# Performance work log

Measured on AMD Instinct MI355X. Metric: run time of the kernel, lower is better.

The kernel has to match this reference:

```python
import jax, jax.numpy as jnp
import numpy as np

E = 512   # embed_dim
H = 512   # hidden_embed_dim
V = 50257 # vocab_size
B = 2048  # batch
EPS = 1e-5


def _layernorm(v, gamma, beta):
    # PyTorch LayerNorm with normalized_shape=(1, H): normalize over last two dims
    m = jnp.mean(v, axis=(-2, -1), keepdims=True)
    var = jnp.var(v, axis=(-2, -1), keepdims=True)
    return (v - m) * jax.lax.rsqrt(var + EPS) * gamma + beta


def setup_inputs() -> dict:
    key = jax.random.key(0)
    ks = jax.random.split(key, 12)
    s_in = 1.0 / np.sqrt(E + H)
    s_h = 1.0 / np.sqrt(H)
    return {
        "x": jax.random.normal(ks[0], (B, 1, E), jnp.float32),
        "h_prev": jax.random.normal(ks[1], (B, 1, H), jnp.float32),
        "W_z": jax.random.normal(ks[2], (H, E + H), jnp.float32) * s_in,
        "b_z": jnp.zeros((H,), jnp.float32),
        "g_z": jnp.ones((1, H), jnp.float32),
        "be_z": jnp.zeros((1, H), jnp.float32),
        "W_r": jax.random.normal(ks[3], (H, E + H), jnp.float32) * s_in,
        "b_r": jnp.zeros((H,), jnp.float32),
        "g_r": jnp.ones((1, H), jnp.float32),
        "be_r": jnp.zeros((1, H), jnp.float32),
        "W_h": jax.random.normal(ks[4], (H, E + H), jnp.float32) * s_in,
        "b_h": jnp.zeros((H,), jnp.float32),
        "g_h": jnp.ones((1, H), jnp.float32),
        "be_h": jnp.zeros((1, H), jnp.float32),
        "W_o": jax.random.normal(ks[5], (V, H), jnp.float32) * s_h,
        "b_o": jnp.zeros((V,), jnp.float32),
    }


def reference(x, h_prev, W_z, b_z, g_z, be_z, W_r, b_r, g_r, be_r,
              W_h, b_h, g_h, be_h, W_o, b_o):
    gru_in = jnp.concatenate([h_prev, x], axis=-1)                 # [B,1,H+E]
    z = jax.nn.sigmoid(_layernorm(gru_in @ W_z.T + b_z, g_z, be_z))
    r = jax.nn.sigmoid(_layernorm(gru_in @ W_r.T + b_r, g_r, be_r))
    cand_in = jnp.concatenate([h_prev * r, x], axis=-1)            # [B,1,H+E]
    h_new = jnp.tanh(_layernorm(cand_in @ W_h.T + b_h, g_h, be_h))
    h_t = (1.0 - z) * h_prev + z * h_new                           # [B,1,H]
    y_t = h_t @ W_o.T + b_o                                        # [B,1,V]
    return (h_t, y_t)
```

## Files before the change

### kernel.cpp

```cpp
#include <hip/hip_runtime.h>
#include <hip/hip_bf16.h>
#include <cstdint>

typedef __bf16 bf16;
typedef bf16 bf16x4 __attribute__((ext_vector_type(4)));
typedef bf16 bf16x8 __attribute__((ext_vector_type(8)));
typedef float f32x4 __attribute__((ext_vector_type(4)));

#define B_  2048
#define E_  512
#define H_  512
#define V_  50257
#define K1_ 1024
#define VPAD_ 50432

#define BAR() __builtin_amdgcn_s_barrier()
#define WAIT_LGKM0() do { asm volatile("s_waitcnt lgkmcnt(0)" ::: "memory"); \
                          __builtin_amdgcn_sched_barrier(0); } while (0)

__device__ __forceinline__ void gload_lds16(const void* g, void* l) {
  __builtin_amdgcn_global_load_lds(
      (const __attribute__((address_space(1))) void*)g,
      (__attribute__((address_space(3))) void*)l, 16, 0, 0);
}

__device__ __forceinline__ float wave_sum(float v) {
#pragma unroll
  for (int o = 32; o > 0; o >>= 1) v += __shfl_xor(v, o, 64);
  return v;
}

__global__ __launch_bounds__(256) void prep_big_kernel(
    const float* __restrict__ hprev, const float* __restrict__ x,
    const float* __restrict__ Wz, const float* __restrict__ Wr,
    const float* __restrict__ Wh, const float* __restrict__ Wo,
    bf16* __restrict__ gin, bf16* __restrict__ wzrh, bf16* __restrict__ wob)
{
  const int i = blockIdx.x * 256 + threadIdx.x;
  constexpr int N1 = B_ * K1_ / 4;
  constexpr int N2 = 1536 * K1_ / 4;
  constexpr int N3 = V_ * 512 / 4;
  if (i < N1) {
    int e = i * 4;
    int m = e >> 10, k = e & 1023;
    const float* src = (k < 512) ? (hprev + (size_t)m * 512 + k)
                                 : (x + (size_t)m * 512 + (k - 512));
    f32x4 v = *reinterpret_cast<const f32x4*>(src);
    bf16x4 t; t[0]=(bf16)v[0]; t[1]=(bf16)v[1]; t[2]=(bf16)v[2]; t[3]=(bf16)v[3];
    *reinterpret_cast<bf16x4*>(gin + e) = t;
  } else if (i < N1 + N2) {
    int e = (i - N1) * 4;
    int which = e >> 19;
    int off = e & ((1 << 19) - 1);
    const float* W = (which == 0) ? Wz : (which == 1) ? Wr : Wh;
    f32x4 v = *reinterpret_cast<const f32x4*>(W + off);
    bf16x4 t; t[0]=(bf16)v[0]; t[1]=(bf16)v[1]; t[2]=(bf16)v[2]; t[3]=(bf16)v[3];
    *reinterpret_cast<bf16x4*>(wzrh + e) = t;
  } else if (i < N1 + N2 + N3) {
    size_t e = (size_t)(i - N1 - N2) * 4;
    f32x4 v = *reinterpret_cast<const f32x4*>(Wo + e);
    bf16x4 t; t[0]=(bf16)v[0]; t[1]=(bf16)v[1]; t[2]=(bf16)v[2]; t[3]=(bf16)v[3];
    *reinterpret_cast<bf16x4*>(wob + e) = t;
  } else {
    size_t e = (size_t)V_ * 512 + (size_t)(i - N1 - N2 - N3) * 4;
    bf16x4 t = {};
    *reinterpret_cast<bf16x4*>(wob + e) = t;
  }
}

__global__ __launch_bounds__(256) void gemm64(
    const bf16* __restrict__ A, const bf16* __restrict__ Bm,
    float* __restrict__ C, int M, int N, int K)
{
  __shared__ bf16 As[2][64 * 64];
  __shared__ bf16 Bs[2][128 * 64];
  const int tid = threadIdx.x;
  const int wid = tid >> 6, lane = tid & 63;
  const int bm = blockIdx.x, bn = blockIdx.y;
  const int wm = (wid >> 1) * 32, wn = (wid & 1) * 64;
  f32x4 acc[2][4] = {};
  const size_t a_row0 = (size_t)bm * 64;
  const size_t b_row0 = (size_t)bn * 128;

  auto STAGE = [&](int buf, int k0) {
#pragma unroll
    for (int i = 0; i < 2; ++i) {
      int base = i * 256 + wid * 64;
      int idx = base + lane;
      int row = idx >> 3;
      int col = ((idx & 7) ^ (row & 7)) << 3;
      gload_lds16(A + (a_row0 + row) * K + (k0 + col), &As[buf][base * 8]);
    }
#pragma unroll
    for (int i = 0; i < 4; ++i) {
      int base = i * 256 + wid * 64;
      int idx = base + lane;
      int row = idx >> 3;
      int col = ((idx & 7) ^ (row & 7)) << 3;
      gload_lds16(Bm + (b_row0 + row) * K + (k0 + col), &Bs[buf][base * 8]);
    }
  };

  auto COMPUTE = [&](int buf) {
#pragma unroll
    for (int kk = 0; kk < 2; ++kk) {
      bf16x8 af[2], bb[4];
#pragma unroll
      for (int i = 0; i < 2; ++i) {
        int ra = wm + i * 16 + (lane & 15);
        int ca = (kk * 32 + (lane >> 4) * 8) ^ ((ra & 7) << 3);
        af[i] = *reinterpret_cast<const bf16x8*>(&As[buf][ra * 64 + ca]);
      }
#pragma unroll
      for (int j = 0; j < 4; ++j) {
        int rb = wn + j * 16 + (lane & 15);
        int cb = (kk * 32 + (lane >> 4) * 8) ^ ((rb & 7) << 3);
        bb[j] = *reinterpret_cast<const bf16x8*>(&Bs[buf][rb * 64 + cb]);
      }
      __builtin_amdgcn_s_setprio(1);
#pragma unroll
      for (int i = 0; i < 2; ++i)
#pragma unroll
        for (int j = 0; j < 4; ++j)
          acc[i][j] = __builtin_amdgcn_mfma_f32_16x16x32_bf16(af[i], bb[j], acc[i][j], 0, 0, 0);
      __builtin_amdgcn_s_setprio(0);
    }
  };

  STAGE(0, 0);
  asm volatile("s_waitcnt vmcnt(0)" ::: "memory");
  __syncthreads();
  const int nt = K >> 6;
  int cur = 0;
  for (int t = 0; t < nt - 1; ++t) {
    STAGE(cur ^ 1, (t + 1) << 6);
    COMPUTE(cur);
    asm volatile("s_waitcnt vmcnt(0)" ::: "memory");
    __syncthreads();
    cur ^= 1;
  }
  COMPUTE(cur);

  const int r0 = (lane >> 4) * 4, cc = lane & 15;
#pragma unroll
  for (int i = 0; i < 2; ++i)
#pragma unroll
    for (int j = 0; j < 4; ++j) {
      int n = bn * 128 + wn + j * 16 + cc;
#pragma unroll
      for (int q = 0; q < 4; ++q) {
        int mm = bm * 64 + wm + i * 16 + r0 + q;
        C[(size_t)mm * N + n] = acc[i][j][q];
      }
    }
}

__global__ __launch_bounds__(256) void ln_zr_kernel(
    const float* __restrict__ zrp,
    const float* __restrict__ bz, const float* __restrict__ br,
    const float* __restrict__ gz, const float* __restrict__ bez,
    const float* __restrict__ gr, const float* __restrict__ ber,
    const float* __restrict__ hprev, const float* __restrict__ x,
    float* __restrict__ zbuf, bf16* __restrict__ cand)
{
  const int m = blockIdx.x, tid = threadIdx.x;
  const int wid = tid >> 6, lane = tid & 63;
  float zv[2], rv[2];
  float s0 = 0, s1 = 0, s2 = 0, s3 = 0;
#pragma unroll
  for (int e = 0; e < 2; ++e) {
    int n = tid + e * 256;
    float a = zrp[(size_t)m * 1024 + n] + bz[n];
    float b = zrp[(size_t)m * 1024 + 512 + n] + br[n];
    zv[e] = a; rv[e] = b;
    s0 += a; s1 += a * a; s2 += b; s3 += b * b;
  }
  s0 = wave_sum(s0); s1 = wave_sum(s1); s2 = wave_sum(s2); s3 = wave_sum(s3);
  __shared__ float red[4][4];
  if (lane == 0) { red[wid][0] = s0; red[wid][1] = s1; red[wid][2] = s2; red[wid][3] = s3; }
  __syncthreads();
  float zs = red[0][0] + red[1][0] + red[2][0] + red[3][0];
  float zq = red[0][1] + red[1][1] + red[2][1] + red[3][1];
  float rs = red[0][2] + red[1][2] + red[2][2] + red[3][2];
  float rq = red[0][3] + red[1][3] + red[2][3] + red[3][3];
  float zm = zs * (1.f / 512.f), zvr = zq * (1.f / 512.f) - zm * zm;
  float rm = rs * (1.f / 512.f), rvr = rq * (1.f / 512.f) - rm * rm;
  float zrs_ = rsqrtf(zvr + 1e-5f), rrs = rsqrtf(rvr + 1e-5f);
#pragma unroll
  for (int e = 0; e < 2; ++e) {
    int n = tid + e * 256;
    float zval = 1.f / (1.f + expf(-((zv[e] - zm) * zrs_ * gz[n] + bez[n])));
    float rval = 1.f / (1.f + expf(-((rv[e] - rm) * rrs * gr[n] + ber[n])));
    zbuf[(size_t)m * 512 + n] = zval;
    cand[(size_t)m * 1024 + n] = (bf16)(hprev[(size_t)m * 512 + n] * rval);
    cand[(size_t)m * 1024 + 512 + n] = (bf16)(x[(size_t)m * 512 + n]);
  }
}

__global__ __launch_bounds__(256) void ln_h_kernel(
    const float* __restrict__ hpre, const float* __restrict__ bh,
    const float* __restrict__ gh, const float* __restrict__ beh,
    const float* __restrict__ zbuf, const float* __restrict__ hprev,
    float* __restrict__ outh, bf16* __restrict__ htb)
{
  const int m = blockIdx.x, tid = threadIdx.x;
  const int wid = tid >> 6, lane = tid & 63;
  float v[2];
  float s0 = 0, s1 = 0;
#pragma unroll
  for (int e = 0; e < 2; ++e) {
    int n = tid + e * 256;
    float a = hpre[(size_t)m * 512 + n] + bh[n];
    v[e] = a; s0 += a; s1 += a * a;
  }
  s0 = wave_sum(s0); s1 = wave_sum(s1);
  __shared__ float red[4][2];
  if (lane == 0) { red[wid][0] = s0; red[wid][1] = s1; }
  __syncthreads();
  float ss = red[0][0] + red[1][0] + red[2][0] + red[3][0];
  float sq = red[0][1] + red[1][1] + red[2][1] + red[3][1];
  float mean = ss * (1.f / 512.f), var = sq * (1.f / 512.f) - mean * mean;
  float rstd = rsqrtf(var + 1e-5f);
#pragma unroll
  for (int e = 0; e < 2; ++e) {
    int n = tid + e * 256;
    float hn = tanhf((v[e] - mean) * rstd * gh[n] + beh[n]);
    float z = zbuf[(size_t)m * 512 + n];
    float ht = (1.f - z) * hprev[(size_t)m * 512 + n] + z * hn;
    outh[(size_t)m * 512 + n] = ht;
    htb[(size_t)m * 512 + n] = (bf16)ht;
  }
}

__global__ __launch_bounds__(512, 2) void gemm_out256(
    const bf16* __restrict__ A, const bf16* __restrict__ Wb,
    const float* __restrict__ bo, float* __restrict__ Y)
{
  __shared__ bf16 lds[2][2][2][128 * 64];
  const int tid = threadIdx.x;
  const int lane = tid & 63;
  const int wid = tid >> 6;
  const int wr = wid >> 2, wc = wid & 3;
  const int hw = blockIdx.x;
  const int logical = (hw & 7) * 197 + (hw >> 3);
  const int bm = logical & 7;
  const int bn = logical >> 3;
  const size_t a_row0 = (size_t)bm * 256;
  const size_t b_row0 = (size_t)bn * 256;
  f32x4 acc[8][4] = {};

  auto STAGE = [&](int p, int op, int h, int ks) {
    const bf16* src = op ? Wb : A;
    const size_t r0 = (op ? b_row0 : a_row0) + h * 128;
    const int k0 = ks << 6;
#pragma unroll
    for (int l = 0; l < 2; ++l) {
      int idx = l * 512 + tid;
      int row = idx >> 3;
      int ch = ((idx & 7) ^ (row & 7)) << 3;
      gload_lds16(src + (r0 + row) * 512 + k0 + ch,
                  &lds[p][op][h][(l * 512 + (tid & ~63)) * 8]);
    }
  };

  auto rdA = [&](int p, int i, int kk) -> bf16x8 {
    int lr = i * 16 + (lane & 15);
    int ch = ((kk * 4 + (lane >> 4)) ^ (lr & 7)) << 3;
    return *reinterpret_cast<const bf16x8*>(&lds[p][0][wr][lr * 64 + ch]);
  };
  auto rdB = [&](int p, int j, int kk) -> bf16x8 {
    int gr = wc * 64 + j * 16 + (lane & 15);
    int lr = gr & 127;
    int ch = ((kk * 4 + (lane >> 4)) ^ (lr & 7)) << 3;
    return *reinterpret_cast<const bf16x8*>(&lds[p][1][wc >> 1][lr * 64 + ch]);
  };

  bf16x8 a0[4][2], a1[4][2], bb0[2][2], bb1[2][2];

  auto MM = [&](bf16x8 (&af)[4][2], bf16x8 (&bf)[2][2], int ib, int jb) {
    __builtin_amdgcn_s_setprio(1);
#pragma unroll
    for (int i = 0; i < 4; ++i)
#pragma unroll
      for (int j = 0; j < 2; ++j)
#pragma unroll
        for (int kk = 0; kk < 2; ++kk)
          acc[ib + i][jb + j] =
              __builtin_amdgcn_mfma_f32_16x16x32_bf16(af[i][kk], bf[j][kk],
                                                      acc[ib + i][jb + j], 0, 0, 0);
    __builtin_amdgcn_s_setprio(0);
  };

  STAGE(0, 0, 0, 0); STAGE(0, 0, 1, 0); STAGE(0, 1, 0, 0); STAGE(0, 1, 1, 0);
  STAGE(1, 0, 0, 1); STAGE(1, 0, 1, 1);
  asm volatile("s_waitcnt vmcnt(4)" ::: "memory");
  BAR();

#pragma unroll 1
  for (int it = 0; it < 4; ++it) {
    const int s = 2 * it;
    const bool pre = (it < 3);
#pragma unroll
    for (int i = 0; i < 4; ++i) { a0[i][0] = rdA(0, i, 0); a0[i][1] = rdA(0, i, 1); }
#pragma unroll
    for (int j = 0; j < 2; ++j) { bb0[j][0] = rdB(0, j, 0); bb0[j][1] = rdB(0, j, 1); }
    STAGE(1, 1, 0, s + 1);
    BAR(); WAIT_LGKM0();
    MM(a0, bb0, 0, 0);
    BAR();
#pragma unroll
    for (int i = 0; i < 4; ++i) { a1[i][0] = rdA(0, 4 + i, 0); a1[i][1] = rdA(0, 4 + i, 1); }
    STAGE(1, 1, 1, s + 1);
    BAR(); WAIT_LGKM0();
    MM(a1, bb0, 4, 0);
    BAR();
#pragma unroll
    for (int j = 0; j < 2; ++j) { bb1[j][0] = rdB(0, 2 + j, 0); bb1[j][1] = rdB(0, 2 + j, 1); }
    if (pre) STAGE(0, 0, 0, s + 2);
    BAR(); WAIT_LGKM0();
    MM(a0, bb1, 0, 2);
    BAR();
    if (pre) { STAGE(0, 1, 0, s + 2);
               asm volatile("s_waitcnt vmcnt(4)" ::: "memory"); }
    else     { asm volatile("s_waitcnt vmcnt(0)" ::: "memory"); }
    BAR();
    MM(a1, bb1, 4, 2);
    BAR();
#pragma unroll
    for (int i = 0; i < 4; ++i) { a0[i][0] = rdA(1, i, 0); a0[i][1] = rdA(1, i, 1); }
#pragma unroll
    for (int j = 0; j < 2; ++j) { bb0[j][0] = rdB(1, j, 0); bb0[j][1] = rdB(1, j, 1); }
    if (pre) STAGE(0, 0, 1, s + 2);
    BAR(); WAIT_LGKM0();
    MM(a0, bb0, 0, 0);
    BAR();
#pragma unroll
    for (int i = 0; i < 4; ++i) { a1[i][0] = rdA(1, 4 + i, 0); a1[i][1] = rdA(1, 4 + i, 1); }
    if (pre) STAGE(0, 1, 1, s + 2);
    BAR(); WAIT_LGKM0();
    MM(a1, bb0, 4, 0);
    BAR();
#pragma unroll
    for (int j = 0; j < 2; ++j) { bb1[j][0] = rdB(1, 2 + j, 0); bb1[j][1] = rdB(1, 2 + j, 1); }
    if (pre) STAGE(1, 0, 0, s + 3);
    BAR(); WAIT_LGKM0();
    MM(a0, bb1, 0, 2);
    BAR();
    if (pre) { STAGE(1, 0, 1, s + 3);
               asm volatile("s_waitcnt vmcnt(4)" ::: "memory"); }
    BAR();
    MM(a1, bb1, 4, 2);
    BAR();
  }

  const int r0q = (lane >> 4) * 4, cc = lane & 15;
  const int rowbase = (int)a_row0 + wr * 128;
  const int colbase = (int)b_row0 + wc * 64;
  float bia[4]; bool val[4];
#pragma unroll
  for (int j = 0; j < 4; ++j) {
    int n = colbase + j * 16 + cc;
    val[j] = (n < V_);
    bia[j] = val[j] ? bo[n] : 0.f;
  }
#pragma unroll
  for (int i = 0; i < 8; ++i) {
#pragma unroll
    for (int q = 0; q < 4; ++q) {
      size_t rowoff = (size_t)(rowbase + i * 16 + r0q + q) * V_;
#pragma unroll
      for (int j = 0; j < 4; ++j) {
        if (val[j]) Y[rowoff + colbase + j * 16 + cc] = acc[i][j][q] + bia[j];
      }
    }
  }
}

__global__ __launch_bounds__(256) void gemm_out_kernel(
    const bf16* __restrict__ A, const float* __restrict__ Wo,
    const float* __restrict__ bo, float* __restrict__ Y)
{
  __shared__ bf16 As[128 * 64];
  __shared__ bf16 Bs[128 * 64];
  constexpr int K = 512;
  const int tid = threadIdx.x;
  const int wid = tid >> 6, lane = tid & 63;
  const int bm = blockIdx.x, bn = blockIdx.y;
  const int wm = (wid >> 1) * 64, wn = (wid & 1) * 64;
  f32x4 acc[4][4] = {};

  for (int k0 = 0; k0 < K; k0 += 64) {
#pragma unroll
    for (int i = 0; i < 4; ++i) {
      int base = i * 256 + wid * 64;
      int idx = base + lane;
      int row = idx >> 3, col = (idx & 7) << 3;
      gload_lds16(A + ((size_t)bm * 128 + row) * K + (k0 + col), &As[base * 8]);
    }
#pragma unroll
    for (int i = 0; i < 8; ++i) {
      int idx = i * 256 + tid;
      int row = idx >> 4;
      int c4 = (idx & 15) * 4;
      int n = bn * 128 + row;
      int nc = (n < V_) ? n : (V_ - 1);
      f32x4 v = *reinterpret_cast<const f32x4*>(Wo + (size_t)nc * K + k0 + c4);
      bf16x4 t; t[0]=(bf16)v[0]; t[1]=(bf16)v[1]; t[2]=(bf16)v[2]; t[3]=(bf16)v[3];
      *reinterpret_cast<bf16x4*>(&Bs[row * 64 + c4]) = t;
    }
    asm volatile("s_waitcnt vmcnt(0)" ::: "memory");
    __syncthreads();
#pragma unroll
    for (int kk = 0; kk < 2; ++kk) {
      bf16x8 af[4], bb[4];
#pragma unroll
      for (int i = 0; i < 4; ++i)
        af[i] = *reinterpret_cast<const bf16x8*>(
            &As[(wm + i * 16 + (lane & 15)) * 64 + kk * 32 + (lane >> 4) * 8]);
#pragma unroll
      for (int j = 0; j < 4; ++j)
        bb[j] = *reinterpret_cast<const bf16x8*>(
            &Bs[(wn + j * 16 + (lane & 15)) * 64 + kk * 32 + (lane >> 4) * 8]);
#pragma unroll
      for (int i = 0; i < 4; ++i)
#pragma unroll
        for (int j = 0; j < 4; ++j)
          acc[i][j] = __builtin_amdgcn_mfma_f32_16x16x32_bf16(af[i], bb[j], acc[i][j], 0, 0, 0);
    }
    __syncthreads();
  }

  const int r0 = (lane >> 4) * 4, cc = lane & 15;
#pragma unroll
  for (int i = 0; i < 4; ++i)
#pragma unroll
    for (int j = 0; j < 4; ++j) {
      int n = bn * 128 + wn + j * 16 + cc;
      if (n < V_) {
        float bia = bo[n];
#pragma unroll
        for (int q = 0; q < 4; ++q) {
          int mm = bm * 128 + wm + i * 16 + r0 + q;
          Y[(size_t)mm * V_ + n] = acc[i][j][q] + bia;
        }
      }
    }
}

__global__ __launch_bounds__(256) void prep_kernel(
    const float* __restrict__ hprev, const float* __restrict__ x,
    const float* __restrict__ Wz, const float* __restrict__ Wr,
    const float* __restrict__ Wh,
    bf16* __restrict__ gin, bf16* __restrict__ wzrh)
{
  const int i = blockIdx.x * 256 + threadIdx.x;
  constexpr int N1 = B_ * K1_ / 4;
  constexpr int N2 = 1536 * K1_ / 4;
  if (i < N1) {
    int e = i * 4;
    int m = e >> 10, k = e & 1023;
    const float* src = (k < 512) ? (hprev + (size_t)m * 512 + k)
                                 : (x + (size_t)m * 512 + (k - 512));
    f32x4 v = *reinterpret_cast<const f32x4*>(src);
    bf16x4 t; t[0]=(bf16)v[0]; t[1]=(bf16)v[1]; t[2]=(bf16)v[2]; t[3]=(bf16)v[3];
    *reinterpret_cast<bf16x4*>(gin + e) = t;
  } else if (i < N1 + N2) {
    int e = (i - N1) * 4;
    int which = e >> 19;
    int off = e & ((1 << 19) - 1);
    const float* W = (which == 0) ? Wz : (which == 1) ? Wr : Wh;
    f32x4 v = *reinterpret_cast<const f32x4*>(W + off);
    bf16x4 t; t[0]=(bf16)v[0]; t[1]=(bf16)v[1]; t[2]=(bf16)v[2]; t[3]=(bf16)v[3];
    *reinterpret_cast<bf16x4*>(wzrh + e) = t;
  }
}

extern "C" void kernel_launch(void* const* d_in, const int* in_sizes, int n_in,
                              void* d_out, int out_size, void* d_ws, size_t ws_size,
                              hipStream_t stream) {
  const float* x     = (const float*)d_in[0];
  const float* hprev = (const float*)d_in[1];
  const float* Wz    = (const float*)d_in[2];
  const float* bz    = (const float*)d_in[3];
  const float* gz    = (const float*)d_in[4];
  const float* bez   = (const float*)d_in[5];
  const float* Wr    = (const float*)d_in[6];
  const float* br    = (const float*)d_in[7];
  const float* gr    = (const float*)d_in[8];
  const float* ber   = (const float*)d_in[9];
  const float* Wh    = (const float*)d_in[10];
  const float* bh    = (const float*)d_in[11];
  const float* gh    = (const float*)d_in[12];
  const float* beh   = (const float*)d_in[13];
  const float* Wo    = (const float*)d_in[14];
  const float* bo    = (const float*)d_in[15];

  float* out_h = (float*)d_out;
  float* out_y = out_h + (size_t)B_ * H_;

  char* ws = (char*)d_ws;
  bf16*  gin  = (bf16*)(ws);
  bf16*  wzrh = (bf16*)(ws + ((size_t)4 << 20));
  float* zrp  = (float*)(ws + ((size_t)7 << 20));
  float* zbuf = (float*)(ws + ((size_t)15 << 20));
  bf16*  cand = (bf16*)(ws + ((size_t)19 << 20));
  float* hpre = (float*)(ws + ((size_t)23 << 20));
  bf16*  htb  = (bf16*)(ws + ((size_t)27 << 20));
  bf16*  wob  = (bf16*)(ws + ((size_t)29 << 20));

  constexpr size_t NEED = ((size_t)29 << 20) + (size_t)VPAD_ * 512 * 2;

  if (ws_size >= NEED) {
    prep_big_kernel<<<28800, 256, 0, stream>>>(hprev, x, Wz, Wr, Wh, Wo, gin, wzrh, wob);
  } else {
    prep_kernel<<<3584, 256, 0, stream>>>(hprev, x, Wz, Wr, Wh, gin, wzrh);
  }

  gemm64<<<dim3(32, 8), 256, 0, stream>>>(gin, wzrh, zrp, B_, 1024, K1_);
  ln_zr_kernel<<<B_, 256, 0, stream>>>(zrp, bz, br, gz, bez, gr, ber, hprev, x, zbuf, cand);
  gemm64<<<dim3(32, 4), 256, 0, stream>>>(cand, wzrh + (size_t)1024 * 1024, hpre, B_, 512, K1_);
  ln_h_kernel<<<B_, 256, 0, stream>>>(hpre, bh, gh, beh, zbuf, hprev, out_h, htb);

  if (ws_size >= NEED) {
    gemm_out256<<<1576, 512, 0, stream>>>(htb, wob, bo, out_y);
  } else {
    gemm_out_kernel<<<dim3(16, 393), 256, 0, stream>>>(htb, Wo, bo, out_y);
  }
}
```

Measured before the change: 317.8 us.

## Overlap W_o bf16 conversion with gate GEMM and LN kernels via extra blocks

The large fp32-to-bf16 conversion of W_o is removed from the prep kernel and split into two halves. One half is done by extra blocks appended to the z/r gate GEMM launch, the other by extra blocks appended to the z/r LayerNorm launch. The aim is to hide this bandwidth-heavy conversion behind the small, underutilising early kernels instead of running it serially up front. The catch is that the added blocks may contend for memory bandwidth and delay the critical-path GEMM and LN work.

```diff
diff --git a/kernel.cpp b/kernel.cpp
--- a/kernel.cpp
+++ b/kernel.cpp
@@ -14,6 +14,10 @@
 #define K1_ 1024
 #define VPAD_ 50432
 
+#define CONV_TOT  6432896
+#define CONV_PAD  6455296
+#define CONV_HALF 3216448
+
 #define BAR() __builtin_amdgcn_s_barrier()
 #define WAIT_LGKM0() do { asm volatile("s_waitcnt lgkmcnt(0)" ::: "memory"); \
                           __builtin_amdgcn_sched_barrier(0); } while (0)
@@ -30,421 +34,11 @@
   return v;
 }
 
-__global__ __launch_bounds__(256) void prep_big_kernel(
-    const float* __restrict__ hprev, const float* __restrict__ x,
-    const float* __restrict__ Wz, const float* __restrict__ Wr,
-    const float* __restrict__ Wh, const float* __restrict__ Wo,
-    bf16* __restrict__ gin, bf16* __restrict__ wzrh, bf16* __restrict__ wob)
-{
-  const int i = blockIdx.x * 256 + threadIdx.x;
-  constexpr int N1 = B_ * K1_ / 4;
-  constexpr int N2 = 1536 * K1_ / 4;
-  constexpr int N3 = V_ * 512 / 4;
-  if (i < N1) {
-    int e = i * 4;
-    int m = e >> 10, k = e & 1023;
-    const float* src = (k < 512) ? (hprev + (size_t)m * 512 + k)
-                                 : (x + (size_t)m * 512 + (k - 512));
-    f32x4 v = *reinterpret_cast<const f32x4*>(src);
-    bf16x4 t; t[0]=(bf16)v[0]; t[1]=(bf16)v[1]; t[2]=(bf16)v[2]; t[3]=(bf16)v[3];
-    *reinterpret_cast<bf16x4*>(gin + e) = t;
-  } else if (i < N1 + N2) {
-    int e = (i - N1) * 4;
-    int which = e >> 19;
-    int off = e & ((1 << 19) - 1);
-    const float* W = (which == 0) ? Wz : (which == 1) ? Wr : Wh;
-    f32x4 v = *reinterpret_cast<const f32x4*>(W + off);
-    bf16x4 t; t[0]=(bf16)v[0]; t[1]=(bf16)v[1]; t[2]=(bf16)v[2]; t[3]=(bf16)v[3];
-    *reinterpret_cast<bf16x4*>(wzrh + e) = t;
-  } else if (i < N1 + N2 + N3) {
-    size_t e = (size_t)(i - N1 - N2) * 4;
-    f32x4 v = *reinterpret_cast<const f32x4*>(Wo + e);
-    bf16x4 t; t[0]=(bf16)v[0]; t[1]=(bf16)v[1]; t[2]=(bf16)v[2]; t[3]=(bf16)v[3];
-    *reinterpret_cast<bf16x4*>(wob + e) = t;
-  } else {
-    size_t e = (size_t)V_ * 512 + (size_t)(i - N1 - N2 - N3) * 4;
-    bf16x4 t = {};
-    *reinterpret_cast<bf16x4*>(wob + e) = t;
-  }
-}
-
-__global__ __launch_bounds__(256) void gemm64(
-    const bf16* __restrict__ A, const bf16* __restrict__ Bm,
-    float* __restrict__ C, int M, int N, int K)
-{
-  __shared__ bf16 As[2][64 * 64];
-  __shared__ bf16 Bs[2][128 * 64];
-  const int tid = threadIdx.x;
-  const int wid = tid >> 6, lane = tid & 63;
-  const int bm = blockIdx.x, bn = blockIdx.y;
-  const int wm = (wid >> 1) * 32, wn = (wid & 1) * 64;
-  f32x4 acc[2][4] = {};
-  const size_t a_row0 = (size_t)bm * 64;
-  const size_t b_row0 = (size_t)bn * 128;
-
-  auto STAGE = [&](int buf, int k0) {
-#pragma unroll
-    for (int i = 0; i < 2; ++i) {
-      int base = i * 256 + wid * 64;
-      int idx = base + lane;
-      int row = idx >> 3;
-      int col = ((idx & 7) ^ (row & 7)) << 3;
-      gload_lds16(A + (a_row0 + row) * K + (k0 + col), &As[buf][base * 8]);
-    }
-#pragma unroll
-    for (int i = 0; i < 4; ++i) {
-      int base = i * 256 + wid * 64;
-      int idx = base + lane;
-      int row = idx >> 3;
-      int col = ((idx & 7) ^ (row & 7)) << 3;
-      gload_lds16(Bm + (b_row0 + row) * K + (k0 + col), &Bs[buf][base * 8]);
-    }
-  };
-
-  auto COMPUTE = [&](int buf) {
-#pragma unroll
-    for (int kk = 0; kk < 2; ++kk) {
-      bf16x8 af[2], bb[4];
-#pragma unroll
-      for (int i = 0; i < 2; ++i) {
-        int ra = wm + i * 16 + (lane & 15);
-        int ca = (kk * 32 + (lane >> 4) * 8) ^ ((ra & 7) << 3);
-        af[i] = *reinterpret_cast<const bf16x8*>(&As[buf][ra * 64 + ca]);
-      }
-#pragma unroll
-      for (int j = 0; j < 4; ++j) {
-        int rb = wn + j * 16 + (lane & 15);
-        int cb = (kk * 32 + (lane >> 4) * 8) ^ ((rb & 7) << 3);
-        bb[j] = *reinterpret_cast<const bf16x8*>(&Bs[buf][rb * 64 + cb]);
-      }
-      __builtin_amdgcn_s_setprio(1);
-#pragma unroll
-      for (int i = 0; i < 2; ++i)
-#pragma unroll
-        for (int j = 0; j < 4; ++j)
-          acc[i][j] = __builtin_amdgcn_mfma_f32_16x16x32_bf16(af[i], bb[j], acc[i][j], 0, 0, 0);
-      __builtin_amdgcn_s_setprio(0);
-    }
-  };
-
-  STAGE(0, 0);
-  asm volatile("s_waitcnt vmcnt(0)" ::: "memory");
-  __syncthreads();
-  const int nt = K >> 6;
-  int cur = 0;
-  for (int t = 0; t < nt - 1; ++t) {
-    STAGE(cur ^ 1, (t + 1) << 6);
-    COMPUTE(cur);
-    asm volatile("s_waitcnt vmcnt(0)" ::: "memory");
-    __syncthreads();
-    cur ^= 1;
-  }
-  COMPUTE(cur);
-
-  const int r0 = (lane >> 4) * 4, cc = lane & 15;
-#pragma unroll
-  for (int i = 0; i < 2; ++i)
-#pragma unroll
-    for (int j = 0; j < 4; ++j) {
-      int n = bn * 128 + wn + j * 16 + cc;
-#pragma unroll
-      for (int q = 0; q < 4; ++q) {
-        int mm = bm * 64 + wm + i * 16 + r0 + q;
-        C[(size_t)mm * N + n] = acc[i][j][q];
-      }
-    }
-}
-
-__global__ __launch_bounds__(256) void ln_zr_kernel(
-    const float* __restrict__ zrp,
-    const float* __restrict__ bz, const float* __restrict__ br,
-    const float* __restrict__ gz, const float* __restrict__ bez,
-    const float* __restrict__ gr, const float* __restrict__ ber,
-    const float* __restrict__ hprev, const float* __restrict__ x,
-    float* __restrict__ zbuf, bf16* __restrict__ cand)
-{
-  const int m = blockIdx.x, tid = threadIdx.x;
-  const int wid = tid >> 6, lane = tid & 63;
-  float zv[2], rv[2];
-  float s0 = 0, s1 = 0, s2 = 0, s3 = 0;
-#pragma unroll
-  for (int e = 0; e < 2; ++e) {
-    int n = tid + e * 256;
-    float a = zrp[(size_t)m * 1024 + n] + bz[n];
-    float b = zrp[(size_t)m * 1024 + 512 + n] + br[n];
-    zv[e] = a; rv[e] = b;
-    s0 += a; s1 += a * a; s2 += b; s3 += b * b;
-  }
-  s0 = wave_sum(s0); s1 = wave_sum(s1); s2 = wave_sum(s2); s3 = wave_sum(s3);
-  __shared__ float red[4][4];
-  if (lane == 0) { red[wid][0] = s0; red[wid][1] = s1; red[wid][2] = s2; red[wid][3] = s3; }
-  __syncthreads();
-  float zs = red[0][0] + red[1][0] + red[2][0] + red[3][0];
-  float zq = red[0][1] + red[1][1] + red[2][1] + red[3][1];
-  float rs = red[0][2] + red[1][2] + red[2][2] + red[3][2];
-  float rq = red[0][3] + red[1][3] + red[2][3] + red[3][3];
-  float zm = zs * (1.f / 512.f), zvr = zq * (1.f / 512.f) - zm * zm;
-  float rm = rs * (1.f / 512.f), rvr = rq * (1.f / 512.f) - rm * rm;
-  float zrs_ = rsqrtf(zvr + 1e-5f), rrs = rsqrtf(rvr + 1e-5f);
-#pragma unroll
-  for (int e = 0; e < 2; ++e) {
-    int n = tid + e * 256;
-    float zval = 1.f / (1.f + expf(-((zv[e] - zm) * zrs_ * gz[n] + bez[n])));
-    float rval = 1.f / (1.f + expf(-((rv[e] - rm) * rrs * gr[n] + ber[n])));
-    zbuf[(size_t)m * 512 + n] = zval;
-    cand[(size_t)m * 1024 + n] = (bf16)(hprev[(size_t)m * 512 + n] * rval);
-    cand[(size_t)m * 1024 + 512 + n] = (bf16)(x[(size_t)m * 512 + n]);
-  }
-}
-
-__global__ __launch_bounds__(256) void ln_h_kernel(
-    const float* __restrict__ hpre, const float* __restrict__ bh,
-    const float* __restrict__ gh, const float* __restrict__ beh,
-    const float* __restrict__ zbuf, const float* __restrict__ hprev,
-    float* __restrict__ outh, bf16* __restrict__ htb)
-{
-  const int m = blockIdx.x, tid = threadIdx.x;
-  const int wid = tid >> 6, lane = tid & 63;
-  float v[2];
-  float s0 = 0, s1 = 0;
-#pragma unroll
-  for (int e = 0; e < 2; ++e) {
-    int n = tid + e * 256;
-    float a = hpre[(size_t)m * 512 + n] + bh[n];
-    v[e] = a; s0 += a; s1 += a * a;
-  }
-  s0 = wave_sum(s0); s1 = wave_sum(s1);
-  __shared__ float red[4][2];
-  if (lane == 0) { red[wid][0] = s0; red[wid][1] = s1; }
-  __syncthreads();
-  float ss = red[0][0] + red[1][0] + red[2][0] + red[3][0];
-  float sq = red[0][1] + red[1][1] + red[2][1] + red[3][1];
-  float mean = ss * (1.f / 512.f), var = sq * (1.f / 512.f) - mean * mean;
-  float rstd = rsqrtf(var + 1e-5f);
-#pragma unroll
-  for (int e = 0; e < 2; ++e) {
-    int n = tid + e * 256;
-    float hn = tanhf((v[e] - mean) * rstd * gh[n] + beh[n]);
-    float z = zbuf[(size_t)m * 512 + n];
-    float ht = (1.f - z) * hprev[(size_t)m * 512 + n] + z * hn;
-    outh[(size_t)m * 512 + n] = ht;
-    htb[(size_t)m * 512 + n] = (bf16)ht;
-  }
-}
-
-__global__ __launch_bounds__(512, 2) void gemm_out256(
-    const bf16* __restrict__ A, const bf16* __restrict__ Wb,
-    const float* __restrict__ bo, float* __restrict__ Y)
-{
-  __shared__ bf16 lds[2][2][2][128 * 64];
-  const int tid = threadIdx.x;
-  const int lane = tid & 63;
-  const int wid = tid >> 6;
-  const int wr = wid >> 2, wc = wid & 3;
-  const int hw = blockIdx.x;
-  const int logical = (hw & 7) * 197 + (hw >> 3);
-  const int bm = logical & 7;
-  const int bn = logical >> 3;
-  const size_t a_row0 = (size_t)bm * 256;
-  const size_t b_row0 = (size_t)bn * 256;
-  f32x4 acc[8][4] = {};
-
-  auto STAGE = [&](int p, int op, int h, int ks) {
-    const bf16* src = op ? Wb : A;
-    const size_t r0 = (op ? b_row0 : a_row0) + h * 128;
-    const int k0 = ks << 6;
-#pragma unroll
-    for (int l = 0; l < 2; ++l) {
-      int idx = l * 512 + tid;
-      int row = idx >> 3;
-      int ch = ((idx & 7) ^ (row & 7)) << 3;
-      gload_lds16(src + (r0 + row) * 512 + k0 + ch,
-                  &lds[p][op][h][(l * 512 + (tid & ~63)) * 8]);
-    }
-  };
-
-  auto rdA = [&](int p, int i, int kk) -> bf16x8 {
-    int lr = i * 16 + (lane & 15);
-    int ch = ((kk * 4 + (lane >> 4)) ^ (lr & 7)) << 3;
-    return *reinterpret_cast<const bf16x8*>(&lds[p][0][wr][lr * 64 + ch]);
-  };
-  auto rdB = [&](int p, int j, int kk) -> bf16x8 {
-    int gr = wc * 64 + j * 16 + (lane & 15);
-    int lr = gr & 127;
-    int ch = ((kk * 4 + (lane >> 4)) ^ (lr & 7)) << 3;
-    return *reinterpret_cast<const bf16x8*>(&lds[p][1][wc >> 1][lr * 64 + ch]);
-  };
-
-  bf16x8 a0[4][2], a1[4][2], bb0[2][2], bb1[2][2];
-
-  auto MM = [&](bf16x8 (&af)[4][2], bf16x8 (&bf)[2][2], int ib, int jb) {
-    __builtin_amdgcn_s_setprio(1);
-#pragma unroll
-    for (int i = 0; i < 4; ++i)
-#pragma unroll
-      for (int j = 0; j < 2; ++j)
-#pragma unroll
-        for (int kk = 0; kk < 2; ++kk)
-          acc[ib + i][jb + j] =
-              __builtin_amdgcn_mfma_f32_16x16x32_bf16(af[i][kk], bf[j][kk],
-                                                      acc[ib + i][jb + j], 0, 0, 0);
-    __builtin_amdgcn_s_setprio(0);
-  };
-
-  STAGE(0, 0, 0, 0); STAGE(0, 0, 1, 0); STAGE(0, 1, 0, 0); STAGE(0, 1, 1, 0);
-  STAGE(1, 0, 0, 1); STAGE(1, 0, 1, 1);
-  asm volatile("s_waitcnt vmcnt(4)" ::: "memory");
-  BAR();
-
-#pragma unroll 1
-  for (int it = 0; it < 4; ++it) {
-    const int s = 2 * it;
-    const bool pre = (it < 3);
-#pragma unroll
-    for (int i = 0; i < 4; ++i) { a0[i][0] = rdA(0, i, 0); a0[i][1] = rdA(0, i, 1); }
-#pragma unroll
-    for (int j = 0; j < 2; ++j) { bb0[j][0] = rdB(0, j, 0); bb0[j][1] = rdB(0, j, 1); }
-    STAGE(1, 1, 0, s + 1);
-    BAR(); WAIT_LGKM0();
-    MM(a0, bb0, 0, 0);
-    BAR();
-#pragma unroll
-    for (int i = 0; i < 4; ++i) { a1[i][0] = rdA(0, 4 + i, 0); a1[i][1] = rdA(0, 4 + i, 1); }
-    STAGE(1, 1, 1, s + 1);
-    BAR(); WAIT_LGKM0();
-    MM(a1, bb0, 4, 0);
-    BAR();
-#pragma unroll
-    for (int j = 0; j < 2; ++j) { bb1[j][0] = rdB(0, 2 + j, 0); bb1[j][1] = rdB(0, 2 + j, 1); }
-    if (pre) STAGE(0, 0, 0, s + 2);
-    BAR(); WAIT_LGKM0();
-    MM(a0, bb1, 0, 2);
-    BAR();
-    if (pre) { STAGE(0, 1, 0, s + 2);
-               asm volatile("s_waitcnt vmcnt(4)" ::: "memory"); }
-    else     { asm volatile("s_waitcnt vmcnt(0)" ::: "memory"); }
-    BAR();
-    MM(a1, bb1, 4, 2);
-    BAR();
-#pragma unroll
-    for (int i = 0; i < 4; ++i) { a0[i][0] = rdA(1, i, 0); a0[i][1] = rdA(1, i, 1); }
-#pragma unroll
-    for (int j = 0; j < 2; ++j) { bb0[j][0] = rdB(1, j, 0); bb0[j][1] = rdB(1, j, 1); }
-    if (pre) STAGE(0, 0, 1, s + 2);
-    BAR(); WAIT_LGKM0();
-    MM(a0, bb0, 0, 0);
-    BAR();
-#pragma unroll
-    for (int i = 0; i < 4; ++i) { a1[i][0] = rdA(1, 4 + i, 0); a1[i][1] = rdA(1, 4 + i, 1); }
-    if (pre) STAGE(0, 1, 1, s + 2);
-    BAR(); WAIT_LGKM0();
-    MM(a1, bb0, 4, 0);
-    BAR();
-#pragma unroll
-    for (int j = 0; j < 2; ++j) { bb1[j][0] = rdB(1, 2 + j, 0); bb1[j][1] = rdB(1, 2 + j, 1); }
-    if (pre) STAGE(1, 0, 0, s + 3);
-    BAR(); WAIT_LGKM0();
-    MM(a0, bb1, 0, 2);
-    BAR();
-    if (pre) { STAGE(1, 0, 1, s + 3);
-               asm volatile("s_waitcnt vmcnt(4)" ::: "memory"); }
-    BAR();
-    MM(a1, bb1, 4, 2);
-    BAR();
-  }
-
-  const int r0q = (lane >> 4) * 4, cc = lane & 15;
-  const int rowbase = (int)a_row0 + wr * 128;
-  const int colbase = (int)b_row0 + wc * 64;
-  float bia[4]; bool val[4];
-#pragma unroll
-  for (int j = 0; j < 4; ++j) {
-    int n = colbase + j * 16 + cc;
-    val[j] = (n < V_);
-    bia[j] = val[j] ? bo[n] : 0.f;
-  }
-#pragma unroll
-  for (int i = 0; i < 8; ++i) {
-#pragma unroll
-    for (int q = 0; q < 4; ++q) {
-      size_t rowoff = (size_t)(rowbase + i * 16 + r0q + q) * V_;
-#pragma unroll
-      for (int j = 0; j < 4; ++j) {
-        if (val[j]) Y[rowoff + colbase + j * 16 + cc] = acc[i][j][q] + bia[j];
-      }
-    }
-  }
-}
-
-__global__ __launch_bounds__(256) void gemm_out_kernel(
-    const bf16* __restrict__ A, const float* __restrict__ Wo,
-    const float* __restrict__ bo, float* __restrict__ Y)
-{
-  __shared__ bf16 As[128 * 64];
-  __shared__ bf16 Bs[128 * 64];
-  constexpr int K = 512;
-  const int tid = threadIdx.x;
-  const int wid = tid >> 6, lane = tid & 63;
-  const int bm = blockIdx.x, bn = blockIdx.y;
-  const int wm = (wid >> 1) * 64, wn = (wid & 1) * 64;
-  f32x4 acc[4][4] = {};
-
-  for (int k0 = 0; k0 < K; k0 += 64) {
-#pragma unroll
-    for (int i = 0; i < 4; ++i) {
-      int base = i * 256 + wid * 64;
-      int idx = base + lane;
-      int row = idx >> 3, col = (idx & 7) << 3;
-      gload_lds16(A + ((size_t)bm * 128 + row) * K + (k0 + col), &As[base * 8]);
-    }
-#pragma unroll
-    for (int i = 0; i < 8; ++i) {
-      int idx = i * 256 + tid;
-      int row = idx >> 4;
-      int c4 = (idx & 15) * 4;
-      int n = bn * 128 + row;
-      int nc = (n < V_) ? n : (V_ - 1);
-      f32x4 v = *reinterpret_cast<const f32x4*>(Wo + (size_t)nc * K + k0 + c4);
-      bf16x4 t; t[0]=(bf16)v[0]; t[1]=(bf16)v[1]; t[2]=(bf16)v[2]; t[3]=(bf16)v[3];
-      *reinterpret_cast<bf16x4*>(&Bs[row * 64 + c4]) = t;
-    }
-    asm volatile("s_waitcnt vmcnt(0)" ::: "memory");
-    __syncthreads();
-#pragma unroll
-    for (int kk = 0; kk < 2; ++kk) {
-      bf16x8 af[4], bb[4];
-#pragma unroll
-      for (int i = 0; i < 4; ++i)
-        af[i] = *reinterpret_cast<const bf16x8*>(
-            &As[(wm + i * 16 + (lane & 15)) * 64 + kk * 32 + (lane >> 4) * 8]);
-#pragma unroll
-      for (int j = 0; j < 4; ++j)
-        bb[j] = *reinterpret_cast<const bf16x8*>(
-            &Bs[(wn + j * 16 + (lane & 15)) * 64 + kk * 32 + (lane >> 4) * 8]);
-#pragma unroll
-      for (int i = 0; i < 4; ++i)
-#pragma unroll
-        for (int j = 0; j < 4; ++j)
-          acc[i][j] = __builtin_amdgcn_mfma_f32_16x16x32_bf16(af[i], bb[j], acc[i][j], 0, 0, 0);
-    }
-    __syncthreads();
-  }
-
-  const int r0 = (lane >> 4) * 4, cc = lane & 15;
-#pragma unroll
-  for (int i = 0; i < 4; ++i)
-#pragma unroll
-    for (int j = 0; j < 4; ++j) {
-      int n = bn * 128 + wn + j * 16 + cc;
-      if (n < V_) {
-        float bia = bo[n];
-#pragma unroll
-        for (int q = 0; q < 4; ++q) {
-          int mm = bm * 128 + wm + i * 16 + r0 + q;
-          Y[(size_t)mm * V_ + n] = acc[i][j][q] + bia;
-        }
-      }
-    }
+__device__ __forceinline__ void cvt_store4(const float* __restrict__ src,
+                                           bf16* __restrict__ dst, size_t e) {
+  f32x4 v = *reinterpret_cast<const f32x4*>(src + e);
+  bf16x4 t; t[0]=(bf16)v[0]; t[1]=(bf16)v[1]; t[2]=(bf16)v[2]; t[3]=(bf16)v[3];
+  *reinterpret_cast<bf16x4*>(dst + e) = t;
 }
 
 __global__ __launch_bounds__(256) void prep_kernel(
@@ -475,6 +69,496 @@
   }
 }
 
+__global__ __launch_bounds__(256) void gemm64_zr(
+    const bf16* __restrict__ A, const bf16* __restrict__ Bm,
+    float* __restrict__ C,
+    const float* __restrict__ Wo, bf16* __restrict__ wob)
+{
+  const int bx = blockIdx.x;
+  const int tid = threadIdx.x;
+  if (bx >= 256) {
+    const size_t cb = bx - 256;
+    for (size_t idx = cb * 256 + tid; idx < CONV_HALF; idx += (size_t)2048 * 256)
+      cvt_store4(Wo, wob, idx * 4);
+    return;
+  }
+  constexpr int N = 1024, K = K1_;
+  __shared__ bf16 As[2][64 * 64];
+  __shared__ bf16 Bs[2][128 * 64];
+  const int wid = tid >> 6, lane = tid & 63;
+  const int bm = bx & 31, bn = bx >> 5;
+  const int wm = (wid >> 1) * 32, wn = (wid & 1) * 64;
+  f32x4 acc[2][4] = {};
+  const size_t a_row0 = (size_t)bm * 64;
+  const size_t b_row0 = (size_t)bn * 128;
+
+  auto STAGE = [&](int buf, int k0) {
+#pragma unroll
+    for (int i = 0; i < 2; ++i) {
+      int base = i * 256 + wid * 64;
+      int idx = base + lane;
+      int row = idx >> 3;
+      int col = ((idx & 7) ^ (row & 7)) << 3;
+      gload_lds16(A + (a_row0 + row) * K + (k0 + col), &As[buf][base * 8]);
+    }
+#pragma unroll
+    for (int i = 0; i < 4; ++i) {
+      int base = i * 256 + wid * 64;
+      int idx = base + lane;
+      int row = idx >> 3;
+      int col = ((idx & 7) ^ (row & 7)) << 3;
+      gload_lds16(Bm + (b_row0 + row) * K + (k0 + col), &Bs[buf][base * 8]);
+    }
+  };
+
+  auto COMPUTE = [&](int buf) {
+#pragma unroll
+    for (int kk = 0; kk < 2; ++kk) {
+      bf16x8 af[2], bb[4];
+#pragma unroll
+      for (int i = 0; i < 2; ++i) {
+        int ra = wm + i * 16 + (lane & 15);
+        int ca = (kk * 32 + (lane >> 4) * 8) ^ ((ra & 7) << 3);
+        af[i] = *reinterpret_cast<const bf16x8*>(&As[buf][ra * 64 + ca]);
+      }
+#pragma unroll
+      for (int j = 0; j < 4; ++j) {
+        int rb = wn + j * 16 + (lane & 15);
+        int cb2 = (kk * 32 + (lane >> 4) * 8) ^ ((rb & 7) << 3);
+        bb[j] = *reinterpret_cast<const bf16x8*>(&Bs[buf][rb * 64 + cb2]);
+      }
+      __builtin_amdgcn_s_setprio(1);
+#pragma unroll
+      for (int i = 0; i < 2; ++i)
+#pragma unroll
+        for (int j = 0; j < 4; ++j)
+          acc[i][j] = __builtin_amdgcn_mfma_f32_16x16x32_bf16(af[i], bb[j], acc[i][j], 0, 0, 0);
+      __builtin_amdgcn_s_setprio(0);
+    }
+  };
+
+  STAGE(0, 0);
+  asm volatile("s_waitcnt vmcnt(0)" ::: "memory");
+  __syncthreads();
+  const int nt = K >> 6;
+  int cur = 0;
+  for (int t = 0; t < nt - 1; ++t) {
+    STAGE(cur ^ 1, (t + 1) << 6);
+    COMPUTE(cur);
+    asm volatile("s_waitcnt vmcnt(0)" ::: "memory");
+    __syncthreads();
+    cur ^= 1;
+  }
+  COMPUTE(cur);
+
+  const int r0 = (lane >> 4) * 4, cc = lane & 15;
+#pragma unroll
+  for (int i = 0; i < 2; ++i)
+#pragma unroll
+    for (int j = 0; j < 4; ++j) {
+      int n = bn * 128 + wn + j * 16 + cc;
+#pragma unroll
+      for (int q = 0; q < 4; ++q) {
+        int mm = bm * 64 + wm + i * 16 + r0 + q;
+        C[(size_t)mm * N + n] = acc[i][j][q];
+      }
+    }
+}
+
+__global__ __launch_bounds__(256) void gemm64(
+    const bf16* __restrict__ A, const bf16* __restrict__ Bm,
+    float* __restrict__ C, int M, int N, int K)
+{
+  __shared__ bf16 As[2][64 * 64];
+  __shared__ bf16 Bs[2][128 * 64];
+  const int tid = threadIdx.x;
+  const int wid = tid >> 6, lane = tid & 63;
+  const int bm = blockIdx.x, bn = blockIdx.y;
+  const int wm = (wid >> 1) * 32, wn = (wid & 1) * 64;
+  f32x4 acc[2][4] = {};
+  const size_t a_row0 = (size_t)bm * 64;
+  const size_t b_row0 = (size_t)bn * 128;
+
+  auto STAGE = [&](int buf, int k0) {
+#pragma unroll
+    for (int i = 0; i < 2; ++i) {
+      int base = i * 256 + wid * 64;
+      int idx = base + lane;
+      int row = idx >> 3;
+      int col = ((idx & 7) ^ (row & 7)) << 3;
+      gload_lds16(A + (a_row0 + row) * K + (k0 + col), &As[buf][base * 8]);
+    }
+#pragma unroll
+    for (int i = 0; i < 4; ++i) {
+      int base = i * 256 + wid * 64;
+      int idx = base + lane;
+      int row = idx >> 3;
+      int col = ((idx & 7) ^ (row & 7)) << 3;
+      gload_lds16(Bm + (b_row0 + row) * K + (k0 + col), &Bs[buf][base * 8]);
+    }
+  };
+
+  auto COMPUTE = [&](int buf) {
+#pragma unroll
+    for (int kk = 0; kk < 2; ++kk) {
+      bf16x8 af[2], bb[4];
+#pragma unroll
+      for (int i = 0; i < 2; ++i) {
+        int ra = wm + i * 16 + (lane & 15);
+        int ca = (kk * 32 + (lane >> 4) * 8) ^ ((ra & 7) << 3);
+        af[i] = *reinterpret_cast<const bf16x8*>(&As[buf][ra * 64 + ca]);
+      }
+#pragma unroll
+      for (int j = 0; j < 4; ++j) {
+        int rb = wn + j * 16 + (lane & 15);
+        int cb = (kk * 32 + (lane >> 4) * 8) ^ ((rb & 7) << 3);
+        bb[j] = *reinterpret_cast<const bf16x8*>(&Bs[buf][rb * 64 + cb]);
+      }
+      __builtin_amdgcn_s_setprio(1);
+#pragma unroll
+      for (int i = 0; i < 2; ++i)
+#pragma unroll
+        for (int j = 0; j < 4; ++j)
+          acc[i][j] = __builtin_amdgcn_mfma_f32_16x16x32_bf16(af[i], bb[j], acc[i][j], 0, 0, 0);
+      __builtin_amdgcn_s_setprio(0);
+    }
+  };
+
+  STAGE(0, 0);
+  asm volatile("s_waitcnt vmcnt(0)" ::: "memory");
+  __syncthreads();
+  const int nt = K >> 6;
+  int cur = 0;
+  for (int t = 0; t < nt - 1; ++t) {
+    STAGE(cur ^ 1, (t + 1) << 6);
+    COMPUTE(cur);
+    asm volatile("s_waitcnt vmcnt(0)" ::: "memory");
+    __syncthreads();
+    cur ^= 1;
+  }
+  COMPUTE(cur);
+
+  const int r0 = (lane >> 4) * 4, cc = lane & 15;
+#pragma unroll
+  for (int i = 0; i < 2; ++i)
+#pragma unroll
+    for (int j = 0; j < 4; ++j) {
+      int n = bn * 128 + wn + j * 16 + cc;
+#pragma unroll
+      for (int q = 0; q < 4; ++q) {
+        int mm = bm * 64 + wm + i * 16 + r0 + q;
+        C[(size_t)mm * N + n] = acc[i][j][q];
+      }
+    }
+}
+
+__global__ __launch_bounds__(256) void ln_zr_kernel(
+    const float* __restrict__ zrp,
+    const float* __restrict__ bz, const float* __restrict__ br,
+    const float* __restrict__ gz, const float* __restrict__ bez,
+    const float* __restrict__ gr, const float* __restrict__ ber,
+    const float* __restrict__ hprev, const float* __restrict__ x,
+    float* __restrict__ zbuf, bf16* __restrict__ cand,
+    const float* __restrict__ Wo, bf16* __restrict__ wob)
+{
+  const int bx = blockIdx.x, tid = threadIdx.x;
+  if (bx >= 2048) {
+    const size_t cb = bx - 2048;
+    for (size_t idx = CONV_HALF + cb * 256 + tid; idx < CONV_PAD;
+         idx += (size_t)2048 * 256) {
+      if (idx < CONV_TOT) {
+        cvt_store4(Wo, wob, idx * 4);
+      } else {
+        bf16x4 t = {};
+        *reinterpret_cast<bf16x4*>(wob + idx * 4) = t;
+      }
+    }
+    return;
+  }
+  const int m = bx;
+  const int wid = tid >> 6, lane = tid & 63;
+  float zv[2], rv[2];
+  float s0 = 0, s1 = 0, s2 = 0, s3 = 0;
+#pragma unroll
+  for (int e = 0; e < 2; ++e) {
+    int n = tid + e * 256;
+    float a = zrp[(size_t)m * 1024 + n] + bz[n];
+    float b = zrp[(size_t)m * 1024 + 512 + n] + br[n];
+    zv[e] = a; rv[e] = b;
+    s0 += a; s1 += a * a; s2 += b; s3 += b * b;
+  }
+  s0 = wave_sum(s0); s1 = wave_sum(s1); s2 = wave_sum(s2); s3 = wave_sum(s3);
+  __shared__ float red[4][4];
+  if (lane == 0) { red[wid][0] = s0; red[wid][1] = s1; red[wid][2] = s2; red[wid][3] = s3; }
+  __syncthreads();
+  float zs = red[0][0] + red[1][0] + red[2][0] + red[3][0];
+  float zq = red[0][1] + red[1][1] + red[2][1] + red[3][1];
+  float rs = red[0][2] + red[1][2] + red[2][2] + red[3][2];
+  float rq = red[0][3] + red[1][3] + red[2][3] + red[3][3];
+  float zm = zs * (1.f / 512.f), zvr = zq * (1.f / 512.f) - zm * zm;
+  float rm = rs * (1.f / 512.f), rvr = rq * (1.f / 512.f) - rm * rm;
+  float zrs_ = rsqrtf(zvr + 1e-5f), rrs = rsqrtf(rvr + 1e-5f);
+#pragma unroll
+  for (int e = 0; e < 2; ++e) {
+    int n = tid + e * 256;
+    float zval = 1.f / (1.f + expf(-((zv[e] - zm) * zrs_ * gz[n] + bez[n])));
+    float rval = 1.f / (1.f + expf(-((rv[e] - rm) * rrs * gr[n] + ber[n])));
+    zbuf[(size_t)m * 512 + n] = zval;
+    cand[(size_t)m * 1024 + n] = (bf16)(hprev[(size_t)m * 512 + n] * rval);
+    cand[(size_t)m * 1024 + 512 + n] = (bf16)(x[(size_t)m * 512 + n]);
+  }
+}
+
+__global__ __launch_bounds__(256) void ln_h_kernel(
+    const float* __restrict__ hpre, const float* __restrict__ bh,
+    const float* __restrict__ gh, const float* __restrict__ beh,
+    const float* __restrict__ zbuf, const float* __restrict__ hprev,
+    float* __restrict__ outh, bf16* __restrict__ htb)
+{
+  const int m = blockIdx.x, tid = threadIdx.x;
+  const int wid = tid >> 6, lane = tid & 63;
+  float v[2];
+  float s0 = 0, s1 = 0;
+#pragma unroll
+  for (int e = 0; e < 2; ++e) {
+    int n = tid + e * 256;
+    float a = hpre[(size_t)m * 512 + n] + bh[n];
+    v[e] = a; s0 += a; s1 += a * a;
+  }
+  s0 = wave_sum(s0); s1 = wave_sum(s1);
+  __shared__ float red[4][2];
+  if (lane == 0) { red[wid][0] = s0; red[wid][1] = s1; }
+  __syncthreads();
+  float ss = red[0][0] + red[1][0] + red[2][0] + red[3][0];
+  float sq = red[0][1] + red[1][1] + red[2][1] + red[3][1];
+  float mean = ss * (1.f / 512.f), var = sq * (1.f / 512.f) - mean * mean;
+  float rstd = rsqrtf(var + 1e-5f);
+#pragma unroll
+  for (int e = 0; e < 2; ++e) {
+    int n = tid + e * 256;
+    float hn = tanhf((v[e] - mean) * rstd * gh[n] + beh[n]);
+    float z = zbuf[(size_t)m * 512 + n];
+    float ht = (1.f - z) * hprev[(size_t)m * 512 + n] + z * hn;
+    outh[(size_t)m * 512 + n] = ht;
+    htb[(size_t)m * 512 + n] = (bf16)ht;
+  }
+}
+
+__global__ __launch_bounds__(512, 2) void gemm_out256(
+    const bf16* __restrict__ A, const bf16* __restrict__ Wb,
+    const float* __restrict__ bo, float* __restrict__ Y)
+{
+  __shared__ bf16 lds[2][2][2][128 * 64];
+  const int tid = threadIdx.x;
+  const int lane = tid & 63;
+  const int wid = tid >> 6;
+  const int wr = wid >> 2, wc = wid & 3;
+  const int hw = blockIdx.x;
+  const int logical = (hw & 7) * 197 + (hw >> 3);
+  const int bm = logical & 7;
+  const int bn = logical >> 3;
+  const size_t a_row0 = (size_t)bm * 256;
+  const size_t b_row0 = (size_t)bn * 256;
+  f32x4 acc[8][4] = {};
+
+  auto STAGE = [&](int p, int op, int h, int ks) {
+    const bf16* src = op ? Wb : A;
+    const size_t r0 = (op ? b_row0 : a_row0) + h * 128;
+    const int k0 = ks << 6;
+#pragma unroll
+    for (int l = 0; l < 2; ++l) {
+      int idx = l * 512 + tid;
+      int row = idx >> 3;
+      int ch = ((idx & 7) ^ (row & 7)) << 3;
+      gload_lds16(src + (r0 + row) * 512 + k0 + ch,
+                  &lds[p][op][h][(l * 512 + (tid & ~63)) * 8]);
+    }
+  };
+
+  auto rdA = [&](int p, int i, int kk) -> bf16x8 {
+    int lr = i * 16 + (lane & 15);
+    int ch = ((kk * 4 + (lane >> 4)) ^ (lr & 7)) << 3;
+    return *reinterpret_cast<const bf16x8*>(&lds[p][0][wr][lr * 64 + ch]);
+  };
+  auto rdB = [&](int p, int j, int kk) -> bf16x8 {
+    int gr = wc * 64 + j * 16 + (lane & 15);
+    int lr = gr & 127;
+    int ch = ((kk * 4 + (lane >> 4)) ^ (lr & 7)) << 3;
+    return *reinterpret_cast<const bf16x8*>(&lds[p][1][wc >> 1][lr * 64 + ch]);
+  };
+
+  bf16x8 a0[4][2], a1[4][2], bb0[2][2], bb1[2][2];
+
+  auto MM = [&](bf16x8 (&af)[4][2], bf16x8 (&bf)[2][2], int ib, int jb) {
+    __builtin_amdgcn_s_setprio(1);
+#pragma unroll
+    for (int i = 0; i < 4; ++i)
+#pragma unroll
+      for (int j = 0; j < 2; ++j)
+#pragma unroll
+        for (int kk = 0; kk < 2; ++kk)
+          acc[ib + i][jb + j] =
+              __builtin_amdgcn_mfma_f32_16x16x32_bf16(af[i][kk], bf[j][kk],
+                                                      acc[ib + i][jb + j], 0, 0, 0);
+    __builtin_amdgcn_s_setprio(0);
+  };
+
+  STAGE(0, 0, 0, 0); STAGE(0, 0, 1, 0); STAGE(0, 1, 0, 0); STAGE(0, 1, 1, 0);
+  STAGE(1, 0, 0, 1); STAGE(1, 0, 1, 1);
+  asm volatile("s_waitcnt vmcnt(4)" ::: "memory");
+  BAR();
+
+#pragma unroll
+  for (int it = 0; it < 4; ++it) {
+    const int s = 2 * it;
+    const bool pre = (it < 3);
+#pragma unroll
+    for (int i = 0; i < 4; ++i) { a0[i][0] = rdA(0, i, 0); a0[i][1] = rdA(0, i, 1); }
+#pragma unroll
+    for (int j = 0; j < 2; ++j) { bb0[j][0] = rdB(0, j, 0); bb0[j][1] = rdB(0, j, 1); }
+    STAGE(1, 1, 0, s + 1);
+    BAR(); WAIT_LGKM0();
+    MM(a0, bb0, 0, 0);
+    BAR();
+#pragma unroll
+    for (int i = 0; i < 4; ++i) { a1[i][0] = rdA(0, 4 + i, 0); a1[i][1] = rdA(0, 4 + i, 1); }
+    STAGE(1, 1, 1, s + 1);
+    BAR(); WAIT_LGKM0();
+    MM(a1, bb0, 4, 0);
+    BAR();
+#pragma unroll
+    for (int j = 0; j < 2; ++j) { bb1[j][0] = rdB(0, 2 + j, 0); bb1[j][1] = rdB(0, 2 + j, 1); }
+    if (pre) STAGE(0, 0, 0, s + 2);
+    BAR(); WAIT_LGKM0();
+    MM(a0, bb1, 0, 2);
+    BAR();
+    if (pre) { STAGE(0, 1, 0, s + 2);
+               asm volatile("s_waitcnt vmcnt(4)" ::: "memory"); }
+    else     { asm volatile("s_waitcnt vmcnt(0)" ::: "memory"); }
+    BAR();
+    MM(a1, bb1, 4, 2);
+    BAR();
+#pragma unroll
+    for (int i = 0; i < 4; ++i) { a0[i][0] = rdA(1, i, 0); a0[i][1] = rdA(1, i, 1); }
+#pragma unroll
+    for (int j = 0; j < 2; ++j) { bb0[j][0] = rdB(1, j, 0); bb0[j][1] = rdB(1, j, 1); }
+    if (pre) STAGE(0, 0, 1, s + 2);
+    BAR(); WAIT_LGKM0();
+    MM(a0, bb0, 0, 0);
+    BAR();
+#pragma unroll
+    for (int i = 0; i < 4; ++i) { a1[i][0] = rdA(1, 4 + i, 0); a1[i][1] = rdA(1, 4 + i, 1); }
+    if (pre) STAGE(0, 1, 1, s + 2);
+    BAR(); WAIT_LGKM0();
+    MM(a1, bb0, 4, 0);
+    BAR();
+#pragma unroll
+    for (int j = 0; j < 2; ++j) { bb1[j][0] = rdB(1, 2 + j, 0); bb1[j][1] = rdB(1, 2 + j, 1); }
+    if (pre) STAGE(1, 0, 0, s + 3);
+    BAR(); WAIT_LGKM0();
+    MM(a0, bb1, 0, 2);
+    BAR();
+    if (pre) { STAGE(1, 0, 1, s + 3);
+               asm volatile("s_waitcnt vmcnt(4)" ::: "memory"); }
+    BAR();
+    MM(a1, bb1, 4, 2);
+    BAR();
+  }
+
+  const int r0q = (lane >> 4) * 4, cc = lane & 15;
+  const int rowbase = (int)a_row0 + wr * 128;
+  const int colbase = (int)b_row0 + wc * 64;
+  float bia[4]; bool val[4];
+#pragma unroll
+  for (int j = 0; j < 4; ++j) {
+    int n = colbase + j * 16 + cc;
+    val[j] = (n < V_);
+    bia[j] = val[j] ? bo[n] : 0.f;
+  }
+#pragma unroll
+  for (int i = 0; i < 8; ++i) {
+#pragma unroll
+    for (int q = 0; q < 4; ++q) {
+      size_t rowoff = (size_t)(rowbase + i * 16 + r0q + q) * V_;
+#pragma unroll
+      for (int j = 0; j < 4; ++j) {
+        if (val[j]) Y[rowoff + colbase + j * 16 + cc] = acc[i][j][q] + bia[j];
+      }
+    }
+  }
+}
+
+__global__ __launch_bounds__(256) void gemm_out_kernel(
+    const bf16* __restrict__ A, const float* __restrict__ Wo,
+    const float* __restrict__ bo, float* __restrict__ Y)
+{
+  __shared__ bf16 As[128 * 64];
+  __shared__ bf16 Bs[128 * 64];
+  constexpr int K = 512;
+  const int tid = threadIdx.x;
+  const int wid = tid >> 6, lane = tid & 63;
+  const int bm = blockIdx.x, bn = blockIdx.y;
+  const int wm = (wid >> 1) * 64, wn = (wid & 1) * 64;
+  f32x4 acc[4][4] = {};
+
+  for (int k0 = 0; k0 < K; k0 += 64) {
+#pragma unroll
+    for (int i = 0; i < 4; ++i) {
+      int base = i * 256 + wid * 64;
+      int idx = base + lane;
+      int row = idx >> 3, col = (idx & 7) << 3;
+      gload_lds16(A + ((size_t)bm * 128 + row) * K + (k0 + col), &As[base * 8]);
+    }
+#pragma unroll
+    for (int i = 0; i < 8; ++i) {
+      int idx = i * 256 + tid;
+      int row = idx >> 4;
+      int c4 = (idx & 15) * 4;
+      int n = bn * 128 + row;
+      int nc = (n < V_) ? n : (V_ - 1);
+      f32x4 v = *reinterpret_cast<const f32x4*>(Wo + (size_t)nc * K + k0 + c4);
+      bf16x4 t; t[0]=(bf16)v[0]; t[1]=(bf16)v[1]; t[2]=(bf16)v[2]; t[3]=(bf16)v[3];
+      *reinterpret_cast<bf16x4*>(&Bs[row * 64 + c4]) = t;
+    }
+    asm volatile("s_waitcnt vmcnt(0)" ::: "memory");
+    __syncthreads();
+#pragma unroll
+    for (int kk = 0; kk < 2; ++kk) {
+      bf16x8 af[4], bb[4];
+#pragma unroll
+      for (int i = 0; i < 4; ++i)
+        af[i] = *reinterpret_cast<const bf16x8*>(
+            &As[(wm + i * 16 + (lane & 15)) * 64 + kk * 32 + (lane >> 4) * 8]);
+#pragma unroll
+      for (int j = 0; j < 4; ++j)
+        bb[j] = *reinterpret_cast<const bf16x8*>(
+            &Bs[(wn + j * 16 + (lane & 15)) * 64 + kk * 32 + (lane >> 4) * 8]);
+#pragma unroll
+      for (int i = 0; i < 4; ++i)
+#pragma unroll
+        for (int j = 0; j < 4; ++j)
+          acc[i][j] = __builtin_amdgcn_mfma_f32_16x16x32_bf16(af[i], bb[j], acc[i][j], 0, 0, 0);
+    }
+    __syncthreads();
+  }
+
+  const int r0 = (lane >> 4) * 4, cc = lane & 15;
+#pragma unroll
+  for (int i = 0; i < 4; ++i)
+#pragma unroll
+    for (int j = 0; j < 4; ++j) {
+      int n = bn * 128 + wn + j * 16 + cc;
+      if (n < V_) {
+        float bia = bo[n];
+#pragma unroll
+        for (int q = 0; q < 4; ++q) {
+          int mm = bm * 128 + wm + i * 16 + r0 + q;
+          Y[(size_t)mm * V_ + n] = acc[i][j][q] + bia;
+        }
+      }
+    }
+}
+
 extern "C" void kernel_launch(void* const* d_in, const int* in_sizes, int n_in,
                               void* d_out, int out_size, void* d_ws, size_t ws_size,
                               hipStream_t stream) {
@@ -509,19 +593,19 @@
   bf16*  wob  = (bf16*)(ws + ((size_t)29 << 20));
 
   constexpr size_t NEED = ((size_t)29 << 20) + (size_t)VPAD_ * 512 * 2;
-
-  if (ws_size >= NEED) {
-    prep_big_kernel<<<28800, 256, 0, stream>>>(hprev, x, Wz, Wr, Wh, Wo, gin, wzrh, wob);
-  } else {
-    prep_kernel<<<3584, 256, 0, stream>>>(hprev, x, Wz, Wr, Wh, gin, wzrh);
-  }
-
-  gemm64<<<dim3(32, 8), 256, 0, stream>>>(gin, wzrh, zrp, B_, 1024, K1_);
-  ln_zr_kernel<<<B_, 256, 0, stream>>>(zrp, bz, br, gz, bez, gr, ber, hprev, x, zbuf, cand);
+  const bool big = (ws_size >= NEED);
+
+  prep_kernel<<<3584, 256, 0, stream>>>(hprev, x, Wz, Wr, Wh, gin, wzrh);
+
+  gemm64_zr<<<big ? 2304 : 256, 256, 0, stream>>>(gin, wzrh, zrp, Wo, wob);
+
+  ln_zr_kernel<<<big ? 4096 : 2048, 256, 0, stream>>>(
+      zrp, bz, br, gz, bez, gr, ber, hprev, x, zbuf, cand, Wo, wob);
+
   gemm64<<<dim3(32, 4), 256, 0, stream>>>(cand, wzrh + (size_t)1024 * 1024, hpre, B_, 512, K1_);
   ln_h_kernel<<<B_, 256, 0, stream>>>(hpre, bh, gh, beh, zbuf, hprev, out_h, htb);
 
-  if (ws_size >= NEED) {
+  if (big) {
     gemm_out256<<<1576, 512, 0, stream>>>(htb, wob, bo, out_y);
   } else {
     gemm_out_kernel<<<dim3(16, 393), 256, 0, stream>>>(htb, Wo, bo, out_y);
```

New measurement: 309.5 us. 2.6% less time.
